# Kernel tuning notes

Measured on AMD Instinct MI355X. Metric: run time of the kernel, lower is better.

## Reference

```python
import jax, jax.numpy as jnp
import numpy as np

DIM = 768
NUM_HEADS = 12
HEAD_DIM = DIM // NUM_HEADS
SCALE = HEAD_DIM ** -0.5


def setup_inputs() -> dict:
    key = jax.random.key(0)
    k1, k2, k3 = jax.random.split(key, 3)
    B, N = 4, 2048
    x = jax.random.normal(k1, (B, N, DIM), dtype=jnp.float32)
    Wqkv = jax.random.normal(k2, (DIM, 3 * DIM), dtype=jnp.float32) * (DIM ** -0.5)
    Wproj = jax.random.normal(k3, (DIM, DIM), dtype=jnp.float32) * (DIM ** -0.5)
    bproj = jnp.zeros((DIM,), dtype=jnp.float32)
    return {"x": x, "Wqkv": Wqkv, "Wproj": Wproj, "bproj": bproj}


def reference(x, Wqkv, Wproj, bproj):
    B, N, C = x.shape
    # qkv: [B, N, 3, H, D] -> split into q, k, v each [B, H, N, D]
    qkv = (x @ Wqkv).reshape(B, N, 3, NUM_HEADS, HEAD_DIM)
    qkv = jnp.transpose(qkv, (2, 0, 3, 1, 4))
    q, k, v = qkv[0], qkv[1], qkv[2]
    attn = jnp.einsum("bhnd,bhmd->bhnm", q, k) * SCALE
    attn = jax.nn.softmax(attn, axis=-1)  # dropout p=0 -> identity
    out = jnp.einsum("bhnm,bhmd->bhnd", attn, v)
    out = jnp.transpose(out, (0, 2, 1, 3)).reshape(B, N, C)
    return out @ Wproj + bproj
```

## Files before the change

kernel.cpp:

```cpp
#include <hip/hip_runtime.h>
#include <math.h>

typedef __bf16 bf16;
typedef __attribute__((ext_vector_type(8))) __bf16 bf16x8;
typedef __attribute__((ext_vector_type(4))) __bf16 bf16x4;
typedef __attribute__((ext_vector_type(4))) float f32x4;

#define NHEADS 12
#define HDIM 64
#define BATCH 4
#define SEQ 2048
#define CDIM 768
#define MTOK (BATCH * SEQ)
#define PERPART ((size_t)MTOK * CDIM)
#define NBH (BATCH * NHEADS)
#define NKB (SEQ / 64)

#define KSCALE 0.18033688011112042f
#define SHIFT 11.54156032f

__device__ static inline void load_lds_16(const void* g, void* l)
{
    __builtin_amdgcn_global_load_lds(
        (const __attribute__((address_space(1))) unsigned int*)g,
        (__attribute__((address_space(3))) unsigned int*)l, 16, 0, 0);
}

__global__ __launch_bounds__(256)
void convert_bf16(const float* __restrict__ in, bf16* __restrict__ out)
{
    const size_t i = ((size_t)blockIdx.x * 256 + threadIdx.x) * 8;
    const float4 v0 = *(const float4*)(in + i);
    const float4 v1 = *(const float4*)(in + i + 4);
    alignas(16) bf16 o[8];
    o[0] = (bf16)v0.x; o[1] = (bf16)v0.y; o[2] = (bf16)v0.z; o[3] = (bf16)v0.w;
    o[4] = (bf16)v1.x; o[5] = (bf16)v1.y; o[6] = (bf16)v1.z; o[7] = (bf16)v1.w;
    *(uint4*)(out + i) = *(const uint4*)o;
}

__global__ __launch_bounds__(256)
void transpose_convert(const float* __restrict__ in, bf16* __restrict__ out,
                       int R, int C)
{
    __shared__ bf16 T[64][65];
    const int r0 = blockIdx.y * 64, c0 = blockIdx.x * 64;
    const int t = threadIdx.x;
    const int ir = t >> 2, ic = (t & 3) * 16;
    #pragma unroll
    for (int e = 0; e < 16; ++e)
        T[ir][ic + e] = (bf16)in[(size_t)(r0 + ir) * C + c0 + ic + e];
    __syncthreads();
    const int oc = t >> 2, orr = (t & 3) * 16;
    alignas(16) bf16 tmp[16];
    #pragma unroll
    for (int e = 0; e < 16; ++e)
        tmp[e] = T[orr + e][oc];
    bf16* dst = out + (size_t)(c0 + oc) * R + r0 + orr;
    *(uint4*)dst       = *(const uint4*)tmp;
    *(uint4*)(dst + 8) = *(const uint4*)(tmp + 8);
}

template<int NCOLS, int MODE>
__global__ __launch_bounds__(256)
void gemm128(const bf16* __restrict__ A, const bf16* __restrict__ Bt,
             const float* __restrict__ bias,
             bf16* __restrict__ qb, bf16* __restrict__ kb, bf16* __restrict__ vtb,
             float* __restrict__ outf)
{
    __shared__ bf16 As[128 * 32];
    __shared__ bf16 Bs[128 * 32];

    const int t    = threadIdx.x;
    const int w    = t >> 6, lane = t & 63;
    const int ln   = lane & 15, quad = lane >> 4;
    const int wr   = w >> 1, wc = w & 1;
    const int m0   = blockIdx.x * 128, n0 = blockIdx.y * 128;

    f32x4 acc[4][4] = {};

    for (int k0 = 0; k0 < CDIM; k0 += 32) {
        #pragma unroll
        for (int i = 0; i < 2; ++i) {
            const int S   = (w * 2 + i) * 64 + lane;
            const int row = S >> 2, st = S & 3;
            const int g   = st ^ (row & 3);
            load_lds_16(A  + (size_t)(m0 + row) * CDIM + k0 + g * 8,
                        &As[(w * 2 + i) * 512]);
            load_lds_16(Bt + (size_t)(n0 + row) * CDIM + k0 + g * 8,
                        &Bs[(w * 2 + i) * 512]);
        }
        __syncthreads();

        bf16x8 af[4], bf_[4];
        #pragma unroll
        for (int mt = 0; mt < 4; ++mt) {
            const int row = wr * 64 + mt * 16 + ln;
            af[mt] = *(const bf16x8*)&As[row * 32 + (quad ^ (row & 3)) * 8];
        }
        #pragma unroll
        for (int nt = 0; nt < 4; ++nt) {
            const int row = wc * 64 + nt * 16 + ln;
            bf_[nt] = *(const bf16x8*)&Bs[row * 32 + (quad ^ (row & 3)) * 8];
        }
        #pragma unroll
        for (int mt = 0; mt < 4; ++mt)
            #pragma unroll
            for (int nt = 0; nt < 4; ++nt)
                acc[mt][nt] = __builtin_amdgcn_mfma_f32_16x16x32_bf16(
                    af[mt], bf_[nt], acc[mt][nt], 0, 0, 0);
        __syncthreads();
    }

    #pragma unroll
    for (int nt = 0; nt < 4; ++nt) {
        const int c = n0 + wc * 64 + nt * 16 + ln;
        if constexpr (MODE == 0) {
            const int p = c / CDIM, rem = c - p * CDIM;
            const int h = rem >> 6, d = rem & 63;
            #pragma unroll
            for (int mt = 0; mt < 4; ++mt) {
                const int row0 = m0 + wr * 64 + mt * 16 + quad * 4;
                const int b = row0 >> 11, nn = row0 & 2047;
                if (p == 0) {
                    bf16* dst = qb + ((size_t)(b * NHEADS + h) * SEQ + nn) * HDIM + d;
                    #pragma unroll
                    for (int r = 0; r < 4; ++r) dst[r * HDIM] = (bf16)acc[mt][nt][r];
                } else if (p == 1) {
                    bf16* dst = kb + ((size_t)(b * NHEADS + h) * SEQ + nn) * HDIM + d;
                    #pragma unroll
                    for (int r = 0; r < 4; ++r) dst[r * HDIM] = (bf16)(acc[mt][nt][r] * KSCALE);
                } else {
                    alignas(8) bf16 pk[4];
                    #pragma unroll
                    for (int r = 0; r < 4; ++r) pk[r] = (bf16)acc[mt][nt][r];
                    const int nn2 = (nn & ~31) + ((nn >> 2) & 3) * 8 + ((nn >> 4) & 1) * 4;
                    *(uint2*)(vtb + ((size_t)(b * NHEADS + h) * HDIM + d) * SEQ + nn2) =
                        *(const uint2*)pk;
                }
            }
        } else {
            const float bv = bias[c];
            #pragma unroll
            for (int mt = 0; mt < 4; ++mt) {
                const int row0 = m0 + wr * 64 + mt * 16 + quad * 4;
                #pragma unroll
                for (int r = 0; r < 4; ++r)
                    outf[(size_t)(row0 + r) * CDIM + c] = acc[mt][nt][r] + bv;
            }
        }
    }
}

__global__ __launch_bounds__(256, 4)
void attn_kernel(const bf16* __restrict__ Qg, const bf16* __restrict__ Kg,
                 const bf16* __restrict__ Vtg, bf16* __restrict__ ao)
{
    __shared__ bf16 Ks[2][64 * 64];
    __shared__ bf16 Vs[2][64 * 64];

    const int virt = (blockIdx.x & 7) * 96 + (blockIdx.x >> 3);
    const int xq   = virt & 15;
    const int bh   = virt >> 4;

    const int t    = threadIdx.x;
    const int w    = t >> 6, lane = t & 63;
    const int ln   = lane & 15, quad = lane >> 4;
    const int q0   = xq * 128;

    const bf16* Qb = Qg  + (size_t)bh * SEQ * HDIM;
    const bf16* Kb = Kg  + (size_t)bh * SEQ * HDIM;
    const bf16* Vb = Vtg + (size_t)bh * HDIM * SEQ;

    bf16x8 qf[2][2];
    #pragma unroll
    for (int qt = 0; qt < 2; ++qt)
        #pragma unroll
        for (int kk = 0; kk < 2; ++kk) {
            const int row = w * 32 + qt * 16 + ln;
            qf[qt][kk] = *(const bf16x8*)(Qb + (size_t)(q0 + row) * HDIM
                                          + (kk * 4 + quad) * 8);
        }

    #pragma unroll
    for (int i = 0; i < 2; ++i) {
        const int S = w * 128 + i * 64 + lane;
        const int row = S >> 3, g = (S & 7) ^ (row & 7);
        load_lds_16(Kb + (size_t)row * HDIM + g * 8, &Ks[0][(w * 2 + i) * 512]);
        load_lds_16(Vb + (size_t)row * SEQ + g * 8,  &Vs[0][(w * 2 + i) * 512]);
    }
    __syncthreads();

    bf16x8 ones;
    #pragma unroll
    for (int e = 0; e < 8; ++e) ones[e] = (bf16)1.0f;

    f32x4 o_acc[2][4] = {};
    f32x4 racc[2] = {};

    for (int kb = 0; kb < NKB; ++kb) {
        if (kb + 1 < NKB) {
            const int nb   = (kb + 1) & 1;
            const int kpos = (kb + 1) * 64;
            #pragma unroll
            for (int i = 0; i < 2; ++i) {
                const int S = w * 128 + i * 64 + lane;
                const int row = S >> 3, g = (S & 7) ^ (row & 7);
                load_lds_16(Kb + (size_t)(kpos + row) * HDIM + g * 8,
                            &Ks[nb][(w * 2 + i) * 512]);
                load_lds_16(Vb + (size_t)row * SEQ + kpos + g * 8,
                            &Vs[nb][(w * 2 + i) * 512]);
            }
        }

        const bf16* Ksb = Ks[kb & 1];
        const bf16* Vsb = Vs[kb & 1];

        #pragma unroll
        for (int p = 0; p < 2; ++p) {
            union { bf16x8 v8; bf16x4 v4[2]; } pf8[2];
            #pragma unroll
            for (int sub = 0; sub < 2; ++sub) {
                const int mt = p * 2 + sub;
                bf16x8 ka[2];
                #pragma unroll
                for (int kk = 0; kk < 2; ++kk) {
                    const int row = mt * 16 + ln;
                    const int g = (kk * 4 + quad) ^ (row & 7);
                    ka[kk] = *(const bf16x8*)&Ksb[row * 64 + g * 8];
                }
                #pragma unroll
                for (int qt = 0; qt < 2; ++qt) {
                    f32x4 a = {-SHIFT, -SHIFT, -SHIFT, -SHIFT};
                    a = __builtin_amdgcn_mfma_f32_16x16x32_bf16(ka[0], qf[qt][0], a, 0, 0, 0);
                    a = __builtin_amdgcn_mfma_f32_16x16x32_bf16(ka[1], qf[qt][1], a, 0, 0, 0);
                    bf16x4 pb = { (bf16)__builtin_amdgcn_exp2f(a[0]),
                                  (bf16)__builtin_amdgcn_exp2f(a[1]),
                                  (bf16)__builtin_amdgcn_exp2f(a[2]),
                                  (bf16)__builtin_amdgcn_exp2f(a[3]) };
                    pf8[qt].v4[sub] = pb;
                }
            }
            #pragma unroll
            for (int qt = 0; qt < 2; ++qt)
                racc[qt] = __builtin_amdgcn_mfma_f32_16x16x32_bf16(
                    pf8[qt].v8, ones, racc[qt], 0, 0, 0);
            #pragma unroll
            for (int dt = 0; dt < 4; ++dt) {
                const int row = dt * 16 + ln;
                const int g = (p * 4 + quad) ^ (row & 7);
                const bf16x8 vvv = *(const bf16x8*)&Vsb[row * 64 + g * 8];
                #pragma unroll
                for (int qt = 0; qt < 2; ++qt)
                    o_acc[qt][dt] = __builtin_amdgcn_mfma_f32_16x16x32_bf16(
                        pf8[qt].v8, vvv, o_acc[qt][dt], 0, 0, 0);
            }
        }
        __syncthreads();
    }

    const int b = bh / NHEADS, h = bh - b * NHEADS;
    bf16* Ao = ao + (size_t)b * SEQ * CDIM + h * HDIM;
    #pragma unroll
    for (int qt = 0; qt < 2; ++qt) {
        float inv[4];
        #pragma unroll
        for (int r = 0; r < 4; ++r) inv[r] = 1.0f / racc[qt][r];
        #pragma unroll
        for (int dt = 0; dt < 4; ++dt) {
            const int d = dt * 16 + ln;
            #pragma unroll
            for (int r = 0; r < 4; ++r) {
                const int q = q0 + w * 32 + qt * 16 + quad * 4 + r;
                Ao[(size_t)q * CDIM + d] = (bf16)(o_acc[qt][dt][r] * inv[r]);
            }
        }
    }
}

extern "C" void kernel_launch(void* const* d_in, const int* in_sizes, int n_in,
                              void* d_out, int out_size, void* d_ws, size_t ws_size,
                              hipStream_t stream)
{
    const float* x     = (const float*)d_in[0];
    const float* Wqkv  = (const float*)d_in[1];
    const float* Wproj = (const float*)d_in[2];
    const float* bproj = (const float*)d_in[3];
    float* out = (float*)d_out;

    bf16* ws   = (bf16*)d_ws;
    bf16* xb   = ws;
    bf16* wqt  = xb  + PERPART;
    bf16* wpt  = wqt + (size_t)3 * CDIM * CDIM;
    bf16* q    = wpt + (size_t)CDIM * CDIM;
    bf16* k    = q   + PERPART;
    bf16* vt   = k   + PERPART;
    bf16* ao   = vt  + PERPART;

    convert_bf16<<<dim3(PERPART / (256 * 8)), 256, 0, stream>>>(x, xb);
    transpose_convert<<<dim3(3 * CDIM / 64, CDIM / 64), 256, 0, stream>>>(
        Wqkv, wqt, CDIM, 3 * CDIM);
    transpose_convert<<<dim3(CDIM / 64, CDIM / 64), 256, 0, stream>>>(
        Wproj, wpt, CDIM, CDIM);

    gemm128<3 * CDIM, 0><<<dim3(MTOK / 128, 3 * CDIM / 128), 256, 0, stream>>>(
        xb, wqt, nullptr, q, k, vt, nullptr);
    attn_kernel<<<dim3(16 * NBH), 256, 0, stream>>>(q, k, vt, ao);
    gemm128<CDIM, 1><<<dim3(MTOK / 128, CDIM / 128), 256, 0, stream>>>(
        ao, wpt, bproj, nullptr, nullptr, nullptr, out);
}
```

Before: 203.9 us.

## Fuse prep kernels, deepen GEMM K-tile to 64, raise MFMA priority in attention

Three preprocessing launches (x conversion and two weight transpose-converts) become one prep kernel that dispatches on block index, removing two launches. The GEMM now stages 64-wide K tiles with an 8-way XOR swizzle, which halves the barrier count per block and doubles LDS use, and it gains a launch-bounds occupancy hint of 3. The attention inner loop wraps its MFMA sections in s_setprio so matrix work is favoured over other waves. The larger LDS footprint may lower occupancy.

```diff
diff --git a/kernel.cpp b/kernel.cpp
--- a/kernel.cpp
+++ b/kernel.cpp
@@ -27,24 +27,34 @@
 }
 
 __global__ __launch_bounds__(256)
-void convert_bf16(const float* __restrict__ in, bf16* __restrict__ out)
-{
-    const size_t i = ((size_t)blockIdx.x * 256 + threadIdx.x) * 8;
-    const float4 v0 = *(const float4*)(in + i);
-    const float4 v1 = *(const float4*)(in + i + 4);
-    alignas(16) bf16 o[8];
-    o[0] = (bf16)v0.x; o[1] = (bf16)v0.y; o[2] = (bf16)v0.z; o[3] = (bf16)v0.w;
-    o[4] = (bf16)v1.x; o[5] = (bf16)v1.y; o[6] = (bf16)v1.z; o[7] = (bf16)v1.w;
-    *(uint4*)(out + i) = *(const uint4*)o;
-}
-
-__global__ __launch_bounds__(256)
-void transpose_convert(const float* __restrict__ in, bf16* __restrict__ out,
-                       int R, int C)
+void prep(const float* __restrict__ x, const float* __restrict__ Wqkv,
+          const float* __restrict__ Wproj,
+          bf16* __restrict__ xb, bf16* __restrict__ wqt, bf16* __restrict__ wpt)
 {
     __shared__ bf16 T[64][65];
-    const int r0 = blockIdx.y * 64, c0 = blockIdx.x * 64;
-    const int t = threadIdx.x;
+    const int bid = blockIdx.x;
+    const int t   = threadIdx.x;
+
+    if (bid < 3072) {
+        const size_t i = ((size_t)bid * 256 + t) * 8;
+        const float4 v0 = *(const float4*)(x + i);
+        const float4 v1 = *(const float4*)(x + i + 4);
+        alignas(16) bf16 o[8];
+        o[0] = (bf16)v0.x; o[1] = (bf16)v0.y; o[2] = (bf16)v0.z; o[3] = (bf16)v0.w;
+        o[4] = (bf16)v1.x; o[5] = (bf16)v1.y; o[6] = (bf16)v1.z; o[7] = (bf16)v1.w;
+        *(uint4*)(xb + i) = *(const uint4*)o;
+        return;
+    }
+
+    const float* in; bf16* outp; int C, bx, by;
+    if (bid < 3072 + 432) {
+        const int b2 = bid - 3072;
+        in = Wqkv; outp = wqt; C = 3 * CDIM; bx = b2 % 36; by = b2 / 36;
+    } else {
+        const int b2 = bid - 3504;
+        in = Wproj; outp = wpt; C = CDIM;    bx = b2 % 12; by = b2 / 12;
+    }
+    const int r0 = by * 64, c0 = bx * 64;
     const int ir = t >> 2, ic = (t & 3) * 16;
     #pragma unroll
     for (int e = 0; e < 16; ++e)
@@ -55,20 +65,20 @@
     #pragma unroll
     for (int e = 0; e < 16; ++e)
         tmp[e] = T[orr + e][oc];
-    bf16* dst = out + (size_t)(c0 + oc) * R + r0 + orr;
+    bf16* dst = outp + (size_t)(c0 + oc) * CDIM + r0 + orr;
     *(uint4*)dst       = *(const uint4*)tmp;
     *(uint4*)(dst + 8) = *(const uint4*)(tmp + 8);
 }
 
 template<int NCOLS, int MODE>
-__global__ __launch_bounds__(256)
+__global__ __launch_bounds__(256, 3)
 void gemm128(const bf16* __restrict__ A, const bf16* __restrict__ Bt,
              const float* __restrict__ bias,
              bf16* __restrict__ qb, bf16* __restrict__ kb, bf16* __restrict__ vtb,
              float* __restrict__ outf)
 {
-    __shared__ bf16 As[128 * 32];
-    __shared__ bf16 Bs[128 * 32];
+    __shared__ bf16 As[128 * 64];
+    __shared__ bf16 Bs[128 * 64];
 
     const int t    = threadIdx.x;
     const int w    = t >> 6, lane = t & 63;
@@ -78,36 +88,38 @@
 
     f32x4 acc[4][4] = {};
 
-    for (int k0 = 0; k0 < CDIM; k0 += 32) {
-        #pragma unroll
-        for (int i = 0; i < 2; ++i) {
-            const int S   = (w * 2 + i) * 64 + lane;
-            const int row = S >> 2, st = S & 3;
-            const int g   = st ^ (row & 3);
+    for (int k0 = 0; k0 < CDIM; k0 += 64) {
+        #pragma unroll
+        for (int i = 0; i < 4; ++i) {
+            const int S   = w * 256 + i * 64 + lane;
+            const int row = S >> 3, g = (S & 7) ^ (row & 7);
             load_lds_16(A  + (size_t)(m0 + row) * CDIM + k0 + g * 8,
-                        &As[(w * 2 + i) * 512]);
+                        &As[(w * 4 + i) * 512]);
             load_lds_16(Bt + (size_t)(n0 + row) * CDIM + k0 + g * 8,
-                        &Bs[(w * 2 + i) * 512]);
+                        &Bs[(w * 4 + i) * 512]);
         }
         __syncthreads();
 
-        bf16x8 af[4], bf_[4];
-        #pragma unroll
-        for (int mt = 0; mt < 4; ++mt) {
-            const int row = wr * 64 + mt * 16 + ln;
-            af[mt] = *(const bf16x8*)&As[row * 32 + (quad ^ (row & 3)) * 8];
-        }
-        #pragma unroll
-        for (int nt = 0; nt < 4; ++nt) {
-            const int row = wc * 64 + nt * 16 + ln;
-            bf_[nt] = *(const bf16x8*)&Bs[row * 32 + (quad ^ (row & 3)) * 8];
-        }
-        #pragma unroll
-        for (int mt = 0; mt < 4; ++mt)
-            #pragma unroll
-            for (int nt = 0; nt < 4; ++nt)
-                acc[mt][nt] = __builtin_amdgcn_mfma_f32_16x16x32_bf16(
-                    af[mt], bf_[nt], acc[mt][nt], 0, 0, 0);
+        #pragma unroll
+        for (int kk = 0; kk < 2; ++kk) {
+            bf16x8 af[4], bf_[4];
+            #pragma unroll
+            for (int mt = 0; mt < 4; ++mt) {
+                const int row = wr * 64 + mt * 16 + ln;
+                af[mt] = *(const bf16x8*)&As[row * 64 + ((kk * 4 + quad) ^ (row & 7)) * 8];
+            }
+            #pragma unroll
+            for (int nt = 0; nt < 4; ++nt) {
+                const int row = wc * 64 + nt * 16 + ln;
+                bf_[nt] = *(const bf16x8*)&Bs[row * 64 + ((kk * 4 + quad) ^ (row & 7)) * 8];
+            }
+            #pragma unroll
+            for (int mt = 0; mt < 4; ++mt)
+                #pragma unroll
+                for (int nt = 0; nt < 4; ++nt)
+                    acc[mt][nt] = __builtin_amdgcn_mfma_f32_16x16x32_bf16(
+                        af[mt], bf_[nt], acc[mt][nt], 0, 0, 0);
+        }
         __syncthreads();
     }
 
@@ -240,6 +252,7 @@
                     pf8[qt].v4[sub] = pb;
                 }
             }
+            __builtin_amdgcn_s_setprio(1);
             #pragma unroll
             for (int qt = 0; qt < 2; ++qt)
                 racc[qt] = __builtin_amdgcn_mfma_f32_16x16x32_bf16(
@@ -254,6 +267,7 @@
                     o_acc[qt][dt] = __builtin_amdgcn_mfma_f32_16x16x32_bf16(
                         pf8[qt].v8, vvv, o_acc[qt][dt], 0, 0, 0);
             }
+            __builtin_amdgcn_s_setprio(0);
         }
         __syncthreads();
     }
@@ -296,11 +310,7 @@
     bf16* vt   = k   + PERPART;
     bf16* ao   = vt  + PERPART;
 
-    convert_bf16<<<dim3(PERPART / (256 * 8)), 256, 0, stream>>>(x, xb);
-    transpose_convert<<<dim3(3 * CDIM / 64, CDIM / 64), 256, 0, stream>>>(
-        Wqkv, wqt, CDIM, 3 * CDIM);
-    transpose_convert<<<dim3(CDIM / 64, CDIM / 64), 256, 0, stream>>>(
-        Wproj, wpt, CDIM, CDIM);
+    prep<<<dim3(3072 + 432 + 144), 256, 0, stream>>>(x, Wqkv, Wproj, xb, wqt, wpt);
 
     gemm128<3 * CDIM, 0><<<dim3(MTOK / 128, 3 * CDIM / 128), 256, 0, stream>>>(
         xb, wqt, nullptr, q, k, vt, nullptr);
```

New measurement: 190.9 us (median of 2 runs). 6.4% less time.
